# Kernel tuning notes

Measured on AMD Instinct MI355X. Metric: run time of the kernel, lower is better.

## Reference

```python
import jax, jax.numpy as jnp
import numpy as np

B, H, W = 4, 256, 256
IN_HSI, IN_MSI, EMBED = 31, 3, 128
R = 2
MAX_FLOW = 2.0
REG_IN = EMBED + EMBED + (2 * R + 1) ** 2 + 1  # 282


def _conv(x, w, b=None, pad=0, groups=1):
    out = jax.lax.conv_general_dilated(
        x, w, (1, 1), [(pad, pad), (pad, pad)],
        dimension_numbers=('NCHW', 'OIHW', 'NCHW'), feature_group_count=groups)
    if b is not None:
        out = out + b[None, :, None, None]
    return out


def _gauss_window(size=9, sigma=1.5):
    c = jnp.arange(size, dtype=jnp.float32) - (size - 1) / 2.0
    g = jnp.exp(-(c ** 2) / (2.0 * sigma ** 2))
    g = g / g.sum()
    return g[:, None] * g[None, :]


def _ssim_map(a, b, win=9):
    # standard gaussian-window SSIM, per-pixel map averaged over channels
    C = a.shape[1]
    w2d = _gauss_window(win)
    k = jnp.broadcast_to(w2d[None, None], (C, 1, win, win))
    pad = win // 2
    dw = lambda t: _conv(t, k, pad=pad, groups=C)
    mu1, mu2 = dw(a), dw(b)
    mu1s, mu2s, mu12 = mu1 * mu1, mu2 * mu2, mu1 * mu2
    s1 = dw(a * a) - mu1s
    s2 = dw(b * b) - mu2s
    s12 = dw(a * b) - mu12
    C1, C2 = 0.01 ** 2, 0.03 ** 2
    m = ((2 * mu12 + C1) * (2 * s12 + C2)) / ((mu1s + mu2s + C1) * (s1 + s2 + C2))
    return m.mean(axis=1)  # (B,H,W)


def _match_mean_std(src, ref, eps=1e-6):
    sm = src.mean(axis=(2, 3), keepdims=True)
    ss = src.std(axis=(2, 3), keepdims=True, ddof=1)  # torch std is unbiased
    rm = ref.mean(axis=(2, 3), keepdims=True)
    rs = ref.std(axis=(2, 3), keepdims=True, ddof=1)
    return (src - sm) / (ss + eps) * rs + rm


def _l2norm(t, eps=1e-12):
    n = jnp.sqrt(jnp.sum(t * t, axis=1, keepdims=True))
    return t / jnp.maximum(n, eps)


def _corr_volume(q, k, r=R):
    _, _, h, w = q.shape
    q = _l2norm(q)
    k = _l2norm(k)
    kp = jnp.pad(k, ((0, 0), (0, 0), (r, r), (r, r)), mode='edge')  # replicate pad
    outs = []
    for dy in range(-r, r + 1):
        for dx in range(-r, r + 1):
            ks = kp[:, :, r + dy:r + dy + h, r + dx:r + dx + w]
            outs.append(jnp.sum(q * ks, axis=1))
    return jnp.stack(outs, axis=1)  # (B, 25, H, W)


def _reflect(coord, size):
    # PyTorch grid_sample reflection, align_corners=False: reflect about -0.5 and size-0.5
    min_ = -0.5
    span = float(size)
    c = jnp.abs(coord - min_)
    extra = jnp.mod(c, span)
    flips = jnp.floor(c / span)
    c = jnp.where(jnp.mod(flips, 2.0) == 0.0, extra + min_, span - extra + min_)
    return jnp.clip(c, 0.0, size - 1.0)


def _warp(img, flow):
    b, c, h, w = img.shape
    gx = (-1.0 + (2.0 * jnp.arange(w, dtype=img.dtype) + 1.0) / w)[None, None, :] + flow[:, 0] * (2.0 / w)
    gy = (-1.0 + (2.0 * jnp.arange(h, dtype=img.dtype) + 1.0) / h)[None, :, None] + flow[:, 1] * (2.0 / h)
    ix = _reflect(((gx + 1.0) * w - 1.0) / 2.0, w)
    iy = _reflect(((gy + 1.0) * h - 1.0) / 2.0, h)
    x0 = jnp.floor(ix)
    y0 = jnp.floor(iy)
    wx = ix - x0
    wy = iy - y0
    x0i = jnp.clip(x0.astype(jnp.int32), 0, w - 1)
    x1i = jnp.clip(x0i + 1, 0, w - 1)
    y0i = jnp.clip(y0.astype(jnp.int32), 0, h - 1)
    y1i = jnp.clip(y0i + 1, 0, h - 1)
    bi = jnp.arange(b)[:, None, None]
    g = lambda yi, xi: img[bi, :, yi, xi]  # (B,H,W,C)
    out = (g(y0i, x0i) * ((1 - wy) * (1 - wx))[..., None]
           + g(y0i, x1i) * ((1 - wy) * wx)[..., None]
           + g(y1i, x0i) * (wy * (1 - wx))[..., None]
           + g(y1i, x1i) * (wy * wx)[..., None])
    return jnp.transpose(out, (0, 3, 1, 2))


def setup_inputs() -> dict:
    key = jax.random.key(0)
    ks = jax.random.split(key, 16)

    def rn(k, shape, fan_in):
        return (jax.random.normal(k, shape, dtype=jnp.float32) / np.sqrt(fan_in)).astype(jnp.float32)

    return {
        'x': jax.random.normal(ks[0], (B, 2 * IN_HSI, H, W), dtype=jnp.float32),
        'y': jax.random.normal(ks[1], (B, IN_MSI, H, W), dtype=jnp.float32),
        'SRF': jax.random.uniform(ks[2], (IN_MSI, IN_HSI), dtype=jnp.float32) / IN_HSI,
        'conv_half_w': rn(ks[3], (IN_HSI, 2 * IN_HSI, 1, 1), 2 * IN_HSI),
        'conv_half_b': jnp.zeros((IN_HSI,), jnp.float32),
        'q_w': rn(ks[4], (EMBED, IN_HSI, 1, 1), IN_HSI),
        'q_b': jnp.zeros((EMBED,), jnp.float32),
        'k_w': rn(ks[5], (EMBED, IN_MSI, 1, 1), IN_MSI),
        'k_b': jnp.zeros((EMBED,), jnp.float32),
        'r1_w': rn(ks[6], (128, REG_IN, 3, 3), REG_IN * 9),
        'r1_b': jnp.zeros((128,), jnp.float32),
        'r2_w': rn(ks[7], (64, 128, 3, 3), 128 * 9),
        'r2_b': jnp.zeros((64,), jnp.float32),
        'r3_w': rn(ks[8], (2, 64, 1, 1), 64) * 0.1,
        'r3_b': jnp.zeros((2,), jnp.float32),
    }


def reference(x, y, SRF, conv_half_w, conv_half_b, q_w, q_b, k_w, k_b,
              r1_w, r1_b, r2_w, r2_b, r3_w, r3_b):
    x = _conv(x, conv_half_w, conv_half_b)
    x_original = x
    srf_w = SRF[:, :, None, None]  # (in_msi, in_hsi, 1, 1)
    x_projected = jnp.clip(_conv(x, srf_w), -1.0, 1.0)
    x_aligned = jnp.clip(_match_mean_std(x_projected, y), -1.0, 1.0)
    ssim_score = _ssim_map(x_aligned, y, 9)
    difficulty = jnp.clip((1.0 - ssim_score)[:, None] / 2.0, 0.0, 1.0)  # (B,1,H,W)
    q = _conv(x, q_w, q_b)
    k = _conv(y, k_w, k_b)
    corr = _corr_volume(q, k, R)
    reg_in = jnp.concatenate([q, k, corr, difficulty], axis=1)
    h1 = jax.nn.leaky_relu(_conv(reg_in, r1_w, r1_b, pad=1), 0.2)
    h2 = jax.nn.leaky_relu(_conv(h1, r2_w, r2_b, pad=1), 0.2)
    flow = jnp.tanh(_conv(h2, r3_w, r3_b)) * MAX_FLOW * difficulty
    return _warp(x_original, flow)
```

## Files before the change

kernel.cpp:

```cpp
#include <hip/hip_runtime.h>
#include <hip/hip_bf16.h>
#include <math.h>


#define HH 256
#define WWI 256
#define HW 65536
#define CH 31
#define CIN2 62
#define CM 3
#define CE 128
#define REGC 288
#define C1S 1e-4f
#define C2S 9e-4f

typedef unsigned short u16;
typedef unsigned int u32;
typedef short bf16x8 __attribute__((ext_vector_type(8)));
typedef float f32x4 __attribute__((ext_vector_type(4)));

__device__ __forceinline__ float blo(u32 u){ return __uint_as_float(u << 16); }
__device__ __forceinline__ float bhi(u32 u){ return __uint_as_float(u & 0xffff0000u); }
__device__ __forceinline__ float b1f(u16 u){ return __uint_as_float(((u32)u) << 16); }
__device__ __forceinline__ u16 f2b(float f){
    u32 u = __float_as_uint(f);
    u32 r = (u + 0x7fffu + ((u >> 16) & 1u)) >> 16;
    return (u16)r;
}
__device__ __forceinline__ f32x4 mfma16(bf16x8 a, bf16x8 b, f32x4 c){
    return __builtin_amdgcn_mfma_f32_16x16x32_bf16(a, b, c, 0, 0, 0);
}
__device__ __forceinline__ float reflectc(float coord, float size){
    float c = fabsf(coord + 0.5f);
    float extra = fmodf(c, size);
    float flips = floorf(c/size);
    float fo = fmodf(flips, 2.0f);
    float r = (fo == 0.0f) ? (extra - 0.5f) : (size - extra - 0.5f);
    return fminf(fmaxf(r, 0.0f), size - 1.0f);
}

__global__ void k_conv_half(const float* __restrict__ x, const float* __restrict__ w,
                            const float* __restrict__ bias, const float* __restrict__ srf,
                            u16* __restrict__ x31, float* __restrict__ xp){
    __shared__ float sw[CH*CIN2];
    __shared__ float sb[CH+1];
    __shared__ float ssrf[CM*CH];
    for(int i=threadIdx.x;i<CH*CIN2;i+=256) sw[i]=w[i];
    for(int i=threadIdx.x;i<CH;i+=256) sb[i]=bias[i];
    for(int i=threadIdx.x;i<CM*CH;i+=256) ssrf[i]=srf[i];
    __syncthreads();
    int pixg = blockIdx.x*256 + threadIdx.x;
    int b = pixg>>16, hw = pixg&65535;
    float acc[CH];
    #pragma unroll
    for(int c=0;c<CH;c++) acc[c]=sb[c];
    for(int ci=0;ci<CIN2;ci++){
        float xv = x[((size_t)(b*CIN2+ci))*HW + hw];
        #pragma unroll
        for(int c=0;c<CH;c++) acc[c] += sw[c*CIN2+ci]*xv;
    }
    u16* o = x31 + (size_t)pixg*32;
    #pragma unroll
    for(int c=0;c<CH;c++) o[c]=f2b(acc[c]);
    o[31]=0;
    #pragma unroll
    for(int m=0;m<CM;m++){
        float a=0.f;
        #pragma unroll
        for(int c=0;c<CH;c++) a += ssrf[m*CH+c]*acc[c];
        a = fminf(fmaxf(a,-1.f),1.f);
        xp[((size_t)(b*CM+m))*HW + hw] = a;
    }
}

__global__ void k_stats1(const float* __restrict__ xp, const float* __restrict__ y,
                         float2* __restrict__ part, int NB){
    int bid = blockIdx.x;
    int p = bid >> 6, c = bid & 63;
    const float* src = (p<3*NB) ? (xp + (size_t)p*HW) : (y + (size_t)(p-3*NB)*HW);
    const float4* s4 = (const float4*)(src + c*1024);
    float4 v = s4[threadIdx.x];
    float s  = v.x + v.y + v.z + v.w;
    float ss = v.x*v.x + v.y*v.y + v.z*v.z + v.w*v.w;
    #pragma unroll
    for(int t=1;t<64;t<<=1){ s += __shfl_xor(s,t); ss += __shfl_xor(ss,t); }
    __shared__ float rs[4], rss[4];
    int wid = threadIdx.x>>6, lane = threadIdx.x&63;
    if(lane==0){ rs[wid]=s; rss[wid]=ss; }
    __syncthreads();
    if(threadIdx.x==0){
        part[bid] = float2{rs[0]+rs[1]+rs[2]+rs[3], rss[0]+rss[1]+rss[2]+rss[3]};
    }
}

__global__ void k_stats2(const float2* __restrict__ part, float* __restrict__ stats){
    int p = blockIdx.x;
    float2 pa = part[p*64 + threadIdx.x];
    float s = pa.x, ss = pa.y;
    #pragma unroll
    for(int t=1;t<64;t<<=1){ s += __shfl_xor(s,t); ss += __shfl_xor(ss,t); }
    if(threadIdx.x==0){
        float mean = s/(float)HW;
        float var = (ss - s*s/(float)HW) / (float)(HW-1);
        stats[p*2]   = mean;
        stats[p*2+1] = sqrtf(fmaxf(var,0.f));
    }
}

__global__ __launch_bounds__(256) void k_ssim(const float* __restrict__ xp,
                                              const float* __restrict__ y,
                                              const float* __restrict__ stats,
                                              float* __restrict__ diff,
                                              u16* __restrict__ regin, int NB){
    __shared__ float sxa[1600];
    __shared__ float sy2[1600];
    __shared__ float hs[5][1280];
    int t = threadIdx.x;
    int bid = blockIdx.x;
    int bb = bid >> 6;
    int s2 = bid & 63;
    int tx = s2 & 7, ty = s2 >> 3;
    float g[9]; float gs = 0.f;
    #pragma unroll
    for(int k=0;k<9;k++){ float cc=(float)(k-4); g[k]=expf(-cc*cc/4.5f); gs+=g[k]; }
    float ginv = 1.f/gs;
    #pragma unroll
    for(int k=0;k<9;k++) g[k] *= ginv;

    float msum[4] = {0.f,0.f,0.f,0.f};
    for(int m=0;m<3;m++){
        int plane = bb*3+m;
        float sm = stats[plane*2],        ssd = stats[plane*2+1];
        float rm = stats[(plane+3*NB)*2], rsd = stats[(plane+3*NB)*2+1];
        const float* xpp = xp + (size_t)plane*HW;
        const float* yp  = y  + (size_t)plane*HW;
        if(m) __syncthreads();
        #pragma unroll
        for(int it=0; it<7; ++it){
            int s = it*256 + t;
            if(s < 1600){
                int rr = s/40, cc = s - rr*40;
                int gy = ty*32-4+rr, gx = tx*32-4+cc;
                float xv=0.f, yv=0.f;
                if(((unsigned)gy<256u)&&((unsigned)gx<256u)){
                    float v = xpp[(gy<<8)+gx];
                    v = (v-sm)/(ssd+1e-6f)*rsd + rm;
                    xv = fminf(fmaxf(v,-1.f),1.f);
                    yv = yp[(gy<<8)+gx];
                }
                sxa[s]=xv; sy2[s]=yv;
            }
        }
        __syncthreads();
        #pragma unroll
        for(int it=0; it<5; ++it){
            int s = it*256 + t;
            int rr = s>>5, cc = s&31;
            int base = rr*40 + cc;
            float s0=0,s1=0,s2v=0,s3=0,s4=0;
            #pragma unroll
            for(int k=0;k<9;k++){
                float gg=g[k];
                float a=sxa[base+k], b=sy2[base+k];
                s0+=gg*a; s1+=gg*b; s2v+=gg*a*a; s3+=gg*b*b; s4+=gg*a*b;
            }
            hs[0][s]=s0; hs[1][s]=s1; hs[2][s]=s2v; hs[3][s]=s3; hs[4][s]=s4;
        }
        __syncthreads();
        #pragma unroll
        for(int it=0; it<4; ++it){
            int s = it*256 + t;
            int rr = s>>5, cc = s&31;
            float v0=0,v1=0,v2=0,v3=0,v4=0;
            #pragma unroll
            for(int k=0;k<9;k++){
                float gg=g[k];
                int idx=(rr+k)*32+cc;
                v0+=gg*hs[0][idx]; v1+=gg*hs[1][idx]; v2+=gg*hs[2][idx];
                v3+=gg*hs[3][idx]; v4+=gg*hs[4][idx];
            }
            float mu1=v0, mu2=v1;
            float mu1s=mu1*mu1, mu2s=mu2*mu2, mu12=mu1*mu2;
            float sg1=v2-mu1s, sg2=v3-mu2s, sg12=v4-mu12;
            msum[it] += (2.f*mu12+C1S)*(2.f*sg12+C2S)
                      / ((mu1s+mu2s+C1S)*(sg1+sg2+C2S));
        }
    }
    #pragma unroll
    for(int it=0; it<4; ++it){
        int s = it*256 + t;
        int rr = s>>5, cc = s&31;
        int pixg = (bb<<16) + ((ty*32+rr)<<8) + (tx*32+cc);
        float d = fminf(fmaxf((1.f-msum[it]*(1.f/3.f))*0.5f,0.f),1.f);
        diff[pixg] = d;
        regin[(size_t)pixg*REGC + 281] = f2b(d);
    }
}

__global__ __launch_bounds__(128) void k_qk(const u16* __restrict__ x31,
                     const float* __restrict__ y,
                     const float* __restrict__ qw, const float* __restrict__ qb,
                     const float* __restrict__ kw, const float* __restrict__ kb,
                     u16* __restrict__ regin){
    __shared__ float sqw[CE*CH];
    __shared__ float skw[CE*CM];
    __shared__ float sqb[CE], skb[CE];
    for(int i=threadIdx.x;i<CE*CH;i+=128) sqw[i]=qw[i];
    for(int i=threadIdx.x;i<CE*CM;i+=128) skw[i]=kw[i];
    if(threadIdx.x<CE){ sqb[threadIdx.x]=qb[threadIdx.x]; skb[threadIdx.x]=kb[threadIdx.x]; }
    __syncthreads();
    int co = threadIdx.x;
    int p0 = blockIdx.x*32;
    float wk0 = skw[co*CM+0], wk1 = skw[co*CM+1], wk2 = skw[co*CM+2];
    for(int pp=0;pp<32;pp++){
        int pixg = p0+pp;
        int b = pixg>>16, hw = pixg&65535;
        const u16* xr = x31 + (size_t)pixg*32;
        float acc = sqb[co];
        #pragma unroll
        for(int c=0;c<CH;c++) acc += sqw[co*CH+c]*b1f(xr[c]);
        u16* rg = regin + (size_t)pixg*REGC;
        rg[co] = f2b(acc);
        float ack = skb[co] + wk0*y[((size_t)(b*CM  ))*HW+hw]
                            + wk1*y[((size_t)(b*CM+1))*HW+hw]
                            + wk2*y[((size_t)(b*CM+2))*HW+hw];
        rg[128+co] = f2b(ack);
        if(co<6) rg[282+co] = 0;
    }
}

__global__ __launch_bounds__(256) void k_corr(const u16* __restrict__ regin,
                                              u16* __restrict__ regout){
    __shared__ uint4 klv[288*16];
    __shared__ float kinvl[288];
    int t = threadIdx.x;
    int half = t & 1, pidx = t >> 1;
    int rb = blockIdx.x;
    int bid = (rb & 7)*(gridDim.x >> 3) + (rb >> 3);
    int bb = bid >> 9;
    int s2 = bid & 511;
    int tx = s2 & 7, ty = s2 >> 3;
    int lw = pidx & 31, lh = pidx >> 5;
    int w = tx*32 + lw;
    int h = ty*4 + lh;
    int pixg = (bb<<16) + (h<<8) + w;

    uint4 q[8];
    const uint4* qp = (const uint4*)(regin + (size_t)pixg*REGC) + half*8;
    #pragma unroll
    for(int i=0;i<8;i++) q[i] = qp[i];
    float sq = 0.f;
    #pragma unroll
    for(int i=0;i<8;i++){
        uint4 v = q[i];
        sq += blo(v.x)*blo(v.x)+bhi(v.x)*bhi(v.x) + blo(v.y)*blo(v.y)+bhi(v.y)*bhi(v.y)
            + blo(v.z)*blo(v.z)+bhi(v.z)*bhi(v.z) + blo(v.w)*blo(v.w)+bhi(v.w)*bhi(v.w);
    }
    sq += __shfl_xor(sq, 1);
    float qn = 1.f/fmaxf(sqrtf(sq),1e-12f);

    #pragma unroll
    for(int it=0; it<18; ++it){
        int s = it*256 + t;
        int rpx = s >> 4, g = s & 15;
        int rr = rpx/36, cc = rpx - rr*36;
        int gy = min(max(ty*4-2+rr,0),255);
        int gx = min(max(tx*32-2+cc,0),255);
        const uint4* src = (const uint4*)(regin + ((size_t)((bb<<16)+(gy<<8)+gx))*REGC + 128);
        klv[rpx*16 + (g ^ (rpx&15))] = src[g];
    }
    __syncthreads();

    #pragma unroll
    for(int it=0; it<3; ++it){
        int item = it*256 + t;
        int px = item>>1, hf = item&1;
        float s = 0.f;
        if(item < 576){
            const uint4* kp = &klv[px*16];
            int sw = px & 15;
            #pragma unroll
            for(int i=0;i<8;i++){
                uint4 kv = kp[(hf*8+i)^sw];
                s += blo(kv.x)*blo(kv.x)+bhi(kv.x)*bhi(kv.x)
                   + blo(kv.y)*blo(kv.y)+bhi(kv.y)*bhi(kv.y)
                   + blo(kv.z)*blo(kv.z)+bhi(kv.z)*bhi(kv.z)
                   + blo(kv.w)*blo(kv.w)+bhi(kv.w)*bhi(kv.w);
            }
        }
        float so = s + __shfl_xor(s,1);
        if(item < 576 && hf==0) kinvl[px] = 1.f/fmaxf(sqrtf(so),1e-12f);
    }
    __syncthreads();

    float res[13];
    #pragma unroll
    for(int dy=-2;dy<=2;dy++){
        #pragma unroll
        for(int dx=-2;dx<=2;dx++){
            int rpx = (lh+2+dy)*36 + (lw+2+dx);
            const uint4* kp = &klv[rpx*16];
            int sw = rpx & 15;
            float s = 0.f;
            #pragma unroll
            for(int i=0;i<8;i++){
                uint4 kv = kp[(half*8 + i) ^ sw];
                uint4 qv = q[i];
                s += blo(qv.x)*blo(kv.x) + bhi(qv.x)*bhi(kv.x);
                s += blo(qv.y)*blo(kv.y) + bhi(qv.y)*bhi(kv.y);
                s += blo(qv.z)*blo(kv.z) + bhi(qv.z)*bhi(kv.z);
                s += blo(qv.w)*blo(kv.w) + bhi(qv.w)*bhi(kv.w);
            }
            s += __shfl_xor(s, 1);
            float cv = s*qn*kinvl[rpx];
            int o = (dy+2)*5 + (dx+2);
            if(o < 13){ if(half==0) res[o] = cv; }
            else      { if(half==1) res[o-13] = cv; }
        }
    }

    u16* rg = regout + (size_t)pixg*REGC + 256;
    if(half==0){
        u16 p[13];
        #pragma unroll
        for(int i=0;i<13;i++) p[i] = f2b(res[i]);
        uint4 v0; u32* v0p = (u32*)&v0;
        #pragma unroll
        for(int i=0;i<4;i++) v0p[i] = (u32)p[2*i] | ((u32)p[2*i+1]<<16);
        *(uint4*)(rg) = v0;
        *(u32*)(rg+8)  = (u32)p[8]  | ((u32)p[9]<<16);
        *(u32*)(rg+10) = (u32)p[10] | ((u32)p[11]<<16);
        rg[12] = p[12];
    } else {
        u16 p[12];
        #pragma unroll
        for(int i=0;i<12;i++) p[i] = f2b(res[i]);
        rg[13] = p[0];
        *(u32*)(rg+14) = (u32)p[1] | ((u32)p[2]<<16);
        uint4 v1; u32* v1p = (u32*)&v1;
        #pragma unroll
        for(int i=0;i<4;i++) v1p[i] = (u32)p[3+2*i] | ((u32)p[4+2*i]<<16);
        *(uint4*)(rg+16) = v1;
        rg[24] = p[11];
    }
}

__global__ void k_wre(const float* __restrict__ w1, const float* __restrict__ w2,
                      u16* __restrict__ w1f, u16* __restrict__ w2f,
                      u16* __restrict__ zpad){
    int i = blockIdx.x*256 + threadIdx.x;
    if(i < 32) zpad[i] = 0;
    if(i < 9*9*128*32){
        int j = i & 7;
        int gg = (i>>3)&3;
        int co = (i>>5)&127;
        int rest = i>>12;
        int kbg = rest%9, tap = rest/9;
        int ci = kbg*32 + gg*8 + j;
        float v = (ci<282) ? w1[((size_t)co*282 + ci)*9 + tap] : 0.f;
        w1f[i] = f2b(v);
    }
    if(i < 9*4*64*32){
        int j = i & 7;
        int gg = (i>>3)&3;
        int co = (i>>5)&63;
        int rest = i>>11;
        int kbg = rest&3, tap = rest>>2;
        int ci = kbg*32 + gg*8 + j;
        w2f[i] = f2b(w2[((size_t)co*128 + ci)*9 + tap]);
    }
}

template<int MF>
__device__ __forceinline__ void ldaM(const uint4* sbuf, int ky, int kx, int kb,
                                     int lane15, int lgrp, bf16x8* ar){
    #pragma unroll
    for(int mf=0;mf<MF;mf++){
        int spx  = (mf&1)*16 + lane15 + kx;
        int srow = (mf>>1) + ky;
        int slot = (srow*34 + spx)*8 + ((kb*4 + lgrp) ^ (spx&7));
        ar[mf] = *(const bf16x8*)&sbuf[slot];
    }
}

template<int NF, int KBGT, int NCO>
__device__ __forceinline__ void ldbN(const u16* __restrict__ wf, int kbg, int tap,
                                     int co0, int lane15, int lgrp, bf16x8* br){
    #pragma unroll
    for(int nf=0;nf<NF;nf++){
        size_t idx = ((size_t)((tap*KBGT + kbg)*NCO + co0 + nf*16 + lane15))*4 + lgrp;
        br[nf] = *(const bf16x8*)(wf + idx*8);
    }
}

template<int MF, int NF, int KBGT, int NCO, int KBI>
__device__ __forceinline__ void conv_steps(const uint4* sbuf, const u16* __restrict__ wf,
                                           int kbgbase, int co0, int lane15, int lgrp,
                                           f32x4 (&acc)[MF][NF]){
    constexpr int NST = 9*KBI;
    #pragma unroll
    for(int s=0;s<NST;s++){
        int ky,kx,kb;
        if(KBI==2){ ky = s/6; kx = (s>>1)%3; kb = s&1; }
        else      { ky = s/3; kx = s%3;      kb = 0;   }
        bf16x8 a[MF];
        bf16x8 b[NF];
        ldaM<MF>(sbuf, ky,kx,kb, lane15, lgrp, a);
        ldbN<NF,KBGT,NCO>(wf, kbgbase+kb, ky*3+kx, co0, lane15, lgrp, b);
        #pragma unroll
        for(int mf=0;mf<MF;mf++)
            #pragma unroll
            for(int nf=0;nf<NF;nf++)
                acc[mf][nf] = mfma16(a[mf], b[nf], acc[mf][nf]);
    }
}

template<int CSTRIDE, int CINTOT, int NCO, int KBGT, int TM, int FUSE>
__global__ __launch_bounds__(128, 1) void k_conv3(const u16* __restrict__ in,
                                                  const u16* __restrict__ wf,
                                                  const float* __restrict__ bias,
                                                  u16* __restrict__ out16,
                                                  float* __restrict__ outf,
                                                  const float* __restrict__ w3,
                                                  const float* __restrict__ b3,
                                                  const float* __restrict__ diff,
                                                  const u16* __restrict__ x31,
                                                  const u16* __restrict__ zpad){
    constexpr int NW = 2;
    constexpr int NF = NCO/(16*NW);
    constexpr int MF = 2*TM;
    constexpr int NCHUNK = (CINTOT + 63)/64;
    constexpr int NTH = NW*64;
    constexpr int SLOTS = (TM+2)*34*8;
    __shared__ uint4 sT[2*SLOTS];
    __shared__ float swf[132];
    int t = threadIdx.x;
    int lane15 = t & 15, lgrp = (t >> 4) & 3;
    int co0 = (t >> 6) * (NCO/NW);
    int rb = blockIdx.x;
    int bid = (rb & 7)*(gridDim.x >> 3) + (rb >> 3);
    int bb = bid >> 9;
    int s2 = bid & 511;
    int tx = s2 & 7, ty = s2 >> 3;
    int row0 = ty*TM, col0 = tx*32;
    const u16* inb  = in + (size_t)bb*HW*CSTRIDE;

    if(FUSE){
        if(t < 128) swf[t] = w3[t];
        if(t < 2)   swf[128+t] = b3[t];
    }

    f32x4 acc[MF][NF];
    #pragma unroll
    for(int nf=0;nf<NF;nf++){
        float bsv = bias[co0 + nf*16 + lane15];
        #pragma unroll
        for(int mf=0;mf<MF;mf++) acc[mf][nf] = f32x4{bsv,bsv,bsv,bsv};
    }

    auto stage = [&](int buf, int kc){
        constexpr int NIT = (SLOTS + NTH - 1)/NTH;
        #pragma unroll
        for(int it=0; it<NIT; ++it){
            int s = it*NTH + t;
            if(s >= SLOTS) continue;
            int srow = s/272, rem = s - srow*272;
            int spx = rem>>3, ggp = rem&7;
            int gg = ggp ^ (spx&7);
            int gy = row0-1+srow, gx = col0-1+spx;
            bool ok = ((unsigned)gy<256u) && ((unsigned)gx<256u);
            const u16* src = ok ? (inb + (size_t)((gy<<8)+gx)*CSTRIDE + kc + gg*8) : zpad;
            __builtin_amdgcn_global_load_lds(
                (const __attribute__((address_space(1))) u32*)src,
                (__attribute__((address_space(3))) u32*)&sT[buf*SLOTS + s],
                16, 0, 0);
        }
    };

    stage(0, 0);
    __syncthreads();

    int cur = 0;
    for(int j=0;j<NCHUNK;j++){
        if(j+1 < NCHUNK) stage(cur^1, (j+1)*64);
        if(CINTOT==288 && j==NCHUNK-1)
            conv_steps<MF,NF,KBGT,NCO,1>(&sT[cur*SLOTS], wf, j*2, co0, lane15, lgrp, acc);
        else
            conv_steps<MF,NF,KBGT,NCO,2>(&sT[cur*SLOTS], wf, j*2, co0, lane15, lgrp, acc);
        if(j+1 < NCHUNK){
            __syncthreads();
            cur ^= 1;
        }
    }

    if(!FUSE){
        u16* outb = out16 + (size_t)bb*HW*NCO;
        #pragma unroll
        for(int mf=0;mf<MF;mf++){
            int prow  = row0 + (mf>>1);
            int pcolb = col0 + (mf&1)*16 + lgrp*4;
            #pragma unroll
            for(int nf=0;nf<NF;nf++){
                int co = co0 + nf*16 + lane15;
                #pragma unroll
                for(int r=0;r<4;r++){
                    int pix = (prow<<8) + pcolb + r;
                    float v = acc[mf][nf][r];
                    v = (v>0.f) ? v : 0.2f*v;
                    outb[(size_t)pix*NCO + co] = f2b(v);
                }
            }
        }
    } else {
        __syncthreads();
        u16* hl = (u16*)sT;
        #pragma unroll
        for(int mf=0;mf<MF;mf++){
            int lrow = mf>>1;
            int lcol = (mf&1)*16 + lgrp*4;
            #pragma unroll
            for(int nf=0;nf<NF;nf++){
                int ch = co0 + nf*16 + lane15;
                int g  = ch>>3, jj = ch&7;
                #pragma unroll
                for(int r=0;r<4;r++){
                    int px = lrow*32 + lcol + r;
                    float v = acc[mf][nf][r];
                    v = (v>0.f) ? v : 0.2f*v;
                    hl[px*64 + ((g ^ (px&7))<<3) + jj] = f2b(v);
                }
            }
        }
        __syncthreads();
        int px = t;
        int h = row0 + (px>>5), w = col0 + (px&31);
        int pixg = (bb<<16) + (h<<8) + w;
        const uint4* hv = (const uint4*)hl;
        float f0 = swf[128], f1 = swf[129];
        #pragma unroll
        for(int i=0;i<8;i++){
            uint4 u = hv[px*8 + (i ^ (px&7))];
            float vv[8] = {blo(u.x),bhi(u.x),blo(u.y),bhi(u.y),
                           blo(u.z),bhi(u.z),blo(u.w),bhi(u.w)};
            int cb = i*8;
            #pragma unroll
            for(int j2=0;j2<8;j2++){ f0 += swf[cb+j2]*vv[j2]; f1 += swf[64+cb+j2]*vv[j2]; }
        }
        float d = diff[pixg];
        f0 = tanhf(f0)*2.0f*d;
        f1 = tanhf(f1)*2.0f*d;
        float ix = reflectc((float)w + f0, 256.f);
        float iy = reflectc((float)h + f1, 256.f);
        float x0 = floorf(ix), y0 = floorf(iy);
        float wx = ix-x0, wy = iy-y0;
        int x0i = min(max((int)x0,0),255);
        int x1i = min(x0i+1,255);
        int y0i = min(max((int)y0,0),255);
        int y1i = min(y0i+1,255);
        const u16* p00 = x31 + ((size_t)((bb<<16)+(y0i<<8)+x0i))*32;
        const u16* p01 = x31 + ((size_t)((bb<<16)+(y0i<<8)+x1i))*32;
        const u16* p10 = x31 + ((size_t)((bb<<16)+(y1i<<8)+x0i))*32;
        const u16* p11 = x31 + ((size_t)((bb<<16)+(y1i<<8)+x1i))*32;
        float w00=(1.f-wy)*(1.f-wx), w01=(1.f-wy)*wx, w10=wy*(1.f-wx), w11=wy*wx;
        float* ob = outf + (size_t)bb*CH*HW + (h<<8) + w;
        #pragma unroll
        for(int c=0;c<CH;c++){
            ob[(size_t)c*HW] = w00*b1f(p00[c]) + w01*b1f(p01[c])
                             + w10*b1f(p10[c]) + w11*b1f(p11[c]);
        }
    }
}

extern "C" void kernel_launch(void* const* d_in, const int* in_sizes, int n_in,
                              void* d_out, int out_size, void* d_ws, size_t ws_size,
                              hipStream_t stream) {
    const float* x    = (const float*)d_in[0];
    const float* y    = (const float*)d_in[1];
    const float* srf  = (const float*)d_in[2];
    const float* chw  = (const float*)d_in[3];
    const float* chb  = (const float*)d_in[4];
    const float* qw   = (const float*)d_in[5];
    const float* qb   = (const float*)d_in[6];
    const float* kw   = (const float*)d_in[7];
    const float* kb   = (const float*)d_in[8];
    const float* w1   = (const float*)d_in[9];
    const float* b1p  = (const float*)d_in[10];
    const float* w2   = (const float*)d_in[11];
    const float* b2p  = (const float*)d_in[12];
    const float* w3   = (const float*)d_in[13];
    const float* b3p  = (const float*)d_in[14];

    struct Arena {
        u16 *x31, *regin, *h1, *w1f, *w2f, *zpad;
        float *xp, *stats, *diff;
        float2 *part;
    };
    auto layout = [&](char* base, int G, Arena* A)->size_t{
        size_t o = 0;
        auto take = [&](size_t sz)->char*{ char* p = base ? base+o : 0; o += (sz+255)&~255ull; return p; };
        Arena tmpA; Arena* P = A ? A : &tmpA;
        P->x31   = (u16*)  take((size_t)G*HW*32*2);
        P->xp    = (float*)take((size_t)G*3*HW*4);
        P->stats = (float*)take(6*4*2*4);
        P->part  = (float2*)take((size_t)6*4*64*8);
        P->diff  = (float*)take((size_t)G*HW*4);
        P->regin = (u16*)  take((size_t)G*HW*REGC*2);
        P->h1    = (u16*)  take((size_t)G*HW*128*2);
        P->w1f   = (u16*)  take((size_t)9*9*128*32*2);
        P->w2f   = (u16*)  take((size_t)9*4*64*32*2);
        P->zpad  = (u16*)  take(64);
        return o;
    };

    int G = 4;
    while(G > 1 && layout(nullptr, G, nullptr) > ws_size) G >>= 1;
    Arena A;
    layout((char*)d_ws, G, &A);

    k_wre<<<1296, 256, 0, stream>>>(w1, w2, A.w1f, A.w2f, A.zpad);

    for(int g0=0; g0<4; g0+=G){
        int NB = G;
        const float* xg  = x + (size_t)g0*CIN2*HW;
        const float* yg  = y + (size_t)g0*CM*HW;
        float* outg      = (float*)d_out + (size_t)g0*CH*HW;

        k_conv_half<<<NB*256,  256, 0, stream>>>(xg, chw, chb, srf, A.x31, A.xp);
        k_stats1   <<<NB*384,  256, 0, stream>>>(A.xp, yg, A.part, NB);
        k_stats2   <<<NB*6,     64, 0, stream>>>(A.part, A.stats);
        k_ssim     <<<NB*64,   256, 0, stream>>>(A.xp, yg, A.stats, A.diff, A.regin, NB);
        k_qk       <<<NB*2048, 128, 0, stream>>>(A.x31, yg, qw, qb, kw, kb, A.regin);
        k_corr     <<<NB*512,  256, 0, stream>>>(A.regin, A.regin);
        k_conv3<288,288,128,9,4,0><<<NB*512, 128, 0, stream>>>(
            A.regin, A.w1f, b1p, A.h1, nullptr, nullptr, nullptr, nullptr, nullptr, A.zpad);
        k_conv3<128,128, 64,4,4,1><<<NB*512, 128, 0, stream>>>(
            A.h1, A.w2f, b2p, nullptr, outg, w3, b3p, A.diff, A.x31, A.zpad);
    }
}
```

Measured before the change: 601.4 us.

## Restructure 3x3 conv kernels to single-wave blocks covering all output channels

Each conv3 block now runs one 64-thread wave that computes every output channel for a 2-row by 32-column tile, instead of two waves splitting the channels over a 4-row tile. The LDS input staging drops from double to single buffering, with an explicit vmcnt wait and no block barriers. The grid doubles and launch bounds move to 64 threads with a minimum of 2 blocks. The aim is to cut barrier cost and LDS footprint and gain more resident blocks, at the cost of losing the overlap between loads and compute within a block and raising per-wave accumulator register pressure.

```diff
diff --git a/kernel.cpp b/kernel.cpp
--- a/kernel.cpp
+++ b/kernel.cpp
@@ -385,17 +385,17 @@
 
 template<int NF, int KBGT, int NCO>
 __device__ __forceinline__ void ldbN(const u16* __restrict__ wf, int kbg, int tap,
-                                     int co0, int lane15, int lgrp, bf16x8* br){
+                                     int lane15, int lgrp, bf16x8* br){
     #pragma unroll
     for(int nf=0;nf<NF;nf++){
-        size_t idx = ((size_t)((tap*KBGT + kbg)*NCO + co0 + nf*16 + lane15))*4 + lgrp;
+        size_t idx = ((size_t)((tap*KBGT + kbg)*NCO + nf*16 + lane15))*4 + lgrp;
         br[nf] = *(const bf16x8*)(wf + idx*8);
     }
 }
 
 template<int MF, int NF, int KBGT, int NCO, int KBI>
 __device__ __forceinline__ void conv_steps(const uint4* sbuf, const u16* __restrict__ wf,
-                                           int kbgbase, int co0, int lane15, int lgrp,
+                                           int kbgbase, int lane15, int lgrp,
                                            f32x4 (&acc)[MF][NF]){
     constexpr int NST = 9*KBI;
     #pragma unroll
@@ -406,7 +406,7 @@
         bf16x8 a[MF];
         bf16x8 b[NF];
         ldaM<MF>(sbuf, ky,kx,kb, lane15, lgrp, a);
-        ldbN<NF,KBGT,NCO>(wf, kbgbase+kb, ky*3+kx, co0, lane15, lgrp, b);
+        ldbN<NF,KBGT,NCO>(wf, kbgbase+kb, ky*3+kx, lane15, lgrp, b);
         #pragma unroll
         for(int mf=0;mf<MF;mf++)
             #pragma unroll
@@ -415,55 +415,51 @@
     }
 }
 
-template<int CSTRIDE, int CINTOT, int NCO, int KBGT, int TM, int FUSE>
-__global__ __launch_bounds__(128, 1) void k_conv3(const u16* __restrict__ in,
-                                                  const u16* __restrict__ wf,
-                                                  const float* __restrict__ bias,
-                                                  u16* __restrict__ out16,
-                                                  float* __restrict__ outf,
-                                                  const float* __restrict__ w3,
-                                                  const float* __restrict__ b3,
-                                                  const float* __restrict__ diff,
-                                                  const u16* __restrict__ x31,
-                                                  const u16* __restrict__ zpad){
-    constexpr int NW = 2;
-    constexpr int NF = NCO/(16*NW);
+template<int CSTRIDE, int CINTOT, int NCO, int KBGT, int FUSE>
+__global__ __launch_bounds__(64, 2) void k_conv3(const u16* __restrict__ in,
+                                                 const u16* __restrict__ wf,
+                                                 const float* __restrict__ bias,
+                                                 u16* __restrict__ out16,
+                                                 float* __restrict__ outf,
+                                                 const float* __restrict__ w3,
+                                                 const float* __restrict__ b3,
+                                                 const float* __restrict__ diff,
+                                                 const u16* __restrict__ x31,
+                                                 const u16* __restrict__ zpad){
+    constexpr int TM = 2;
+    constexpr int NF = NCO/16;
     constexpr int MF = 2*TM;
     constexpr int NCHUNK = (CINTOT + 63)/64;
-    constexpr int NTH = NW*64;
     constexpr int SLOTS = (TM+2)*34*8;
-    __shared__ uint4 sT[2*SLOTS];
+    __shared__ uint4 sT[SLOTS];
     __shared__ float swf[132];
     int t = threadIdx.x;
-    int lane15 = t & 15, lgrp = (t >> 4) & 3;
-    int co0 = (t >> 6) * (NCO/NW);
+    int lane15 = t & 15, lgrp = t >> 4;
     int rb = blockIdx.x;
     int bid = (rb & 7)*(gridDim.x >> 3) + (rb >> 3);
-    int bb = bid >> 9;
-    int s2 = bid & 511;
+    int bb = bid >> 10;
+    int s2 = bid & 1023;
     int tx = s2 & 7, ty = s2 >> 3;
     int row0 = ty*TM, col0 = tx*32;
-    const u16* inb  = in + (size_t)bb*HW*CSTRIDE;
+    const u16* inb = in + (size_t)bb*HW*CSTRIDE;
 
     if(FUSE){
-        if(t < 128) swf[t] = w3[t];
-        if(t < 2)   swf[128+t] = b3[t];
+        for(int i=t;i<128;i+=64) swf[i] = w3[i];
+        if(t < 2) swf[128+t] = b3[t];
     }
 
     f32x4 acc[MF][NF];
     #pragma unroll
     for(int nf=0;nf<NF;nf++){
-        float bsv = bias[co0 + nf*16 + lane15];
+        float bsv = bias[nf*16 + lane15];
         #pragma unroll
         for(int mf=0;mf<MF;mf++) acc[mf][nf] = f32x4{bsv,bsv,bsv,bsv};
     }
 
-    auto stage = [&](int buf, int kc){
-        constexpr int NIT = (SLOTS + NTH - 1)/NTH;
-        #pragma unroll
-        for(int it=0; it<NIT; ++it){
-            int s = it*NTH + t;
-            if(s >= SLOTS) continue;
+    auto stage = [&](int kc){
+        #pragma unroll
+        for(int it=0; it<17; ++it){
+            int s = it*64 + t;
             int srow = s/272, rem = s - srow*272;
             int spx = rem>>3, ggp = rem&7;
             int gg = ggp ^ (spx&7);
@@ -472,25 +468,18 @@
             const u16* src = ok ? (inb + (size_t)((gy<<8)+gx)*CSTRIDE + kc + gg*8) : zpad;
             __builtin_amdgcn_global_load_lds(
                 (const __attribute__((address_space(1))) u32*)src,
-                (__attribute__((address_space(3))) u32*)&sT[buf*SLOTS + s],
+                (__attribute__((address_space(3))) u32*)&sT[s],
                 16, 0, 0);
         }
     };
 
-    stage(0, 0);
-    __syncthreads();
-
-    int cur = 0;
     for(int j=0;j<NCHUNK;j++){
-        if(j+1 < NCHUNK) stage(cur^1, (j+1)*64);
+        stage(j*64);
+        asm volatile("s_waitcnt vmcnt(0)" ::: "memory");
         if(CINTOT==288 && j==NCHUNK-1)
-            conv_steps<MF,NF,KBGT,NCO,1>(&sT[cur*SLOTS], wf, j*2, co0, lane15, lgrp, acc);
+            conv_steps<MF,NF,KBGT,NCO,1>(sT, wf, j*2, lane15, lgrp, acc);
         else
-            conv_steps<MF,NF,KBGT,NCO,2>(&sT[cur*SLOTS], wf, j*2, co0, lane15, lgrp, acc);
-        if(j+1 < NCHUNK){
-            __syncthreads();
-            cur ^= 1;
-        }
+            conv_steps<MF,NF,KBGT,NCO,2>(sT, wf, j*2, lane15, lgrp, acc);
     }
 
     if(!FUSE){
@@ -501,7 +490,7 @@
             int pcolb = col0 + (mf&1)*16 + lgrp*4;
             #pragma unroll
             for(int nf=0;nf<NF;nf++){
-                int co = co0 + nf*16 + lane15;
+                int co = nf*16 + lane15;
                 #pragma unroll
                 for(int r=0;r<4;r++){
                     int pix = (prow<<8) + pcolb + r;
@@ -520,7 +509,7 @@
             int lcol = (mf&1)*16 + lgrp*4;
             #pragma unroll
             for(int nf=0;nf<NF;nf++){
-                int ch = co0 + nf*16 + lane15;
+                int ch = nf*16 + lane15;
                 int g  = ch>>3, jj = ch&7;
                 #pragma unroll
                 for(int r=0;r<4;r++){
@@ -631,9 +620,9 @@
         k_ssim     <<<NB*64,   256, 0, stream>>>(A.xp, yg, A.stats, A.diff, A.regin, NB);
         k_qk       <<<NB*2048, 128, 0, stream>>>(A.x31, yg, qw, qb, kw, kb, A.regin);
         k_corr     <<<NB*512,  256, 0, stream>>>(A.regin, A.regin);
-        k_conv3<288,288,128,9,4,0><<<NB*512, 128, 0, stream>>>(
+        k_conv3<288,288,128,9,0><<<NB*1024, 64, 0, stream>>>(
             A.regin, A.w1f, b1p, A.h1, nullptr, nullptr, nullptr, nullptr, nullptr, A.zpad);
-        k_conv3<128,128, 64,4,4,1><<<NB*512, 128, 0, stream>>>(
+        k_conv3<128,128, 64,4,1><<<NB*1024, 64, 0, stream>>>(
             A.h1, A.w2f, b2p, nullptr, outg, w3, b3p, A.diff, A.x31, A.zpad);
     }
 }
```

Result: slower. 947.9 us (+57.6%).
